# Optimization experiments

Hardware: AMD Instinct MI355X
Metric: run time of the kernel (lower is better)

The kernel has to match this reference:

```python
import jax, jax.numpy as jnp
import numpy as np

NB_USERS = 100000
NB_MOVIES = 20000
K = 64
N = 2000000
MAX_RATING = 5.0


def setup_inputs() -> dict:
    key = jax.random.key(0)
    ks = jax.random.split(key, 8)
    return {
        "x_users": jnp.arange(NB_USERS, dtype=jnp.int32),  # every user queried once -> original's user filter is identity
        "x_movies": jax.random.randint(ks[0], (NB_USERS,), 0, NB_MOVIES),
        "data_users": jax.random.randint(ks[1], (N,), 0, NB_USERS),
        "data_movies": jax.random.randint(ks[2], (N,), 0, NB_MOVIES),
        "data_ratings": jax.random.uniform(ks[3], (N,), dtype=jnp.float32) * MAX_RATING,
        "movies_features": jax.random.normal(ks[4], (NB_MOVIES, K), dtype=jnp.float32),
        "W_r": jax.random.normal(ks[5], (K, 1), dtype=jnp.float32) * 0.1,
        "b_r": jnp.zeros((K,), dtype=jnp.float32),
        "W_c": jax.random.normal(ks[6], (K, K), dtype=jnp.float32) * 0.1,
        "b_c": jnp.zeros((K,), dtype=jnp.float32),
        "w_out": jax.random.normal(ks[7], (1, 1), dtype=jnp.float32),
        "b_out": jnp.zeros((1,), dtype=jnp.float32),
    }


def reference(x_users, x_movies, data_users, data_movies, data_ratings,
              movies_features, W_r, b_r, W_c, b_c, w_out, b_out):
    # movies_ratings_func: Linear(1,k) + sigmoid on normalized ratings
    ratings = jax.nn.sigmoid((data_ratings[:, None] / MAX_RATING) @ W_r.T + b_r)  # [N,k]
    # combined_func: Linear(k,k) + sigmoid on (gathered movie feats * rating emb)
    rbm = jax.nn.sigmoid((movies_features[data_movies] * ratings) @ W_c.T + b_c)  # [N,k]
    # scatter-add aggregate per user
    rating_by_user = jax.ops.segment_sum(rbm, data_users, num_segments=NB_USERS)  # [U,k]
    nb_ratings = jax.ops.segment_sum(jnp.ones((N,), dtype=rbm.dtype), data_users,
                                     num_segments=NB_USERS)  # [U]
    # ignore_if_seen=True path (faithful, including rbm indexed by movie id as in original)
    rating_by_user = rating_by_user.at[x_users].add(-rbm[x_movies])
    nb_ratings = nb_ratings.at[x_users].set(jnp.maximum(jnp.float32(1.0), nb_ratings[x_users] - 1.0))
    user_features = rating_by_user[x_users] / nb_ratings[x_users][:, None]  # [B,k]
    movie_features = movies_features[x_movies]  # [B,k]
    r = (movie_features * user_features).mean(-1, keepdims=True)  # [B,1]
    r = (r @ w_out.T + b_out) * MAX_RATING  # result_func then *max_rating
    return r.reshape(-1)
```

## Files before the change

### kernel.cpp

```cpp
#include <hip/hip_runtime.h>

#define NB_USERS 100000
#define NB_MOVIES 20000
#define KDIM 64
#define NPTS 2000000
#define RQ_LEVELS 8192
#define UPB 128
#define NBUCK 782
#define CHUNK 8192
#define NCHUNK ((NPTS + CHUNK - 1) / CHUNK)
#define BCAP 3584
#define LOG2E 1.44269504088896f

#define MF_N (NB_MOVIES * KDIM)
#define RT_N ((RQ_LEVELS + 1) * KDIM)

typedef _Float16 f16x8 __attribute__((ext_vector_type(8)));
typedef float    f32x4 __attribute__((ext_vector_type(4)));

__device__ __forceinline__ float sigmoidf(float z) {
    return 1.0f / (1.0f + __expf(-z));
}
__device__ __forceinline__ float sigmoid_w(float w) {
    return __builtin_amdgcn_rcpf(1.0f + __builtin_amdgcn_exp2f(w));
}

__global__ __launch_bounds__(256) void prep_kernel(
    const float* __restrict__ mf, const float* __restrict__ W_r,
    const float* __restrict__ b_r, const float* __restrict__ W_c,
    _Float16* __restrict__ mf16, _Float16* __restrict__ rtab16,
    _Float16* __restrict__ wcfrag)
{
    const int idx = blockIdx.x * 256 + threadIdx.x;
    if (idx < MF_N) {
        mf16[idx] = (_Float16)mf[idx];
    } else if (idx < MF_N + RT_N) {
        const int i = idx - MF_N;
        const int q = i >> 6, k = i & 63;
        rtab16[i] = (_Float16)sigmoidf(fmaf((float)q * (1.0f / RQ_LEVELS), W_r[k], b_r[k]));
    } else if (idx < MF_N + RT_N + 512) {
        const int i = idx - MF_N - RT_N;
        const int ntkt = i >> 6;
        const int nt = ntkt >> 1, kt = ntkt & 1;
        const int lane = i & 63;
        const float* src = &W_c[(nt * 16 + (lane & 15)) * KDIM + kt * 32 + (lane >> 4) * 8];
        _Float16* dst = wcfrag + (size_t)ntkt * 512 + lane * 8;
        #pragma unroll
        for (int e = 0; e < 8; ++e) dst[e] = (_Float16)(src[e] * -LOG2E);
    }
}

__global__ __launch_bounds__(1024) void bucket_hist_kernel(
    const int* __restrict__ du, int* __restrict__ bhist)
{
    __shared__ int h[NBUCK];
    for (int b = threadIdx.x; b < NBUCK; b += 1024) h[b] = 0;
    __syncthreads();
    int i = blockIdx.x * 1024 + threadIdx.x;
    const int stride = gridDim.x * 1024;
    for (; i < NPTS; i += stride) atomicAdd(&h[du[i] >> 7], 1);
    __syncthreads();
    for (int b = threadIdx.x; b < NBUCK; b += 1024)
        if (h[b]) atomicAdd(&bhist[b], h[b]);
}

__global__ __launch_bounds__(256) void bscan_kernel(
    const int* __restrict__ bhist, int* __restrict__ bstart, int* __restrict__ bcursor)
{
    __shared__ int scn[256];
    const int t = threadIdx.x;
    int c[4];
    int s = 0;
    #pragma unroll
    for (int j = 0; j < 4; ++j) {
        const int idx = t * 4 + j;
        c[j] = (idx < NBUCK) ? bhist[idx] : 0;
        s += c[j];
    }
    scn[t] = s;
    __syncthreads();
    for (int d = 1; d < 256; d <<= 1) {
        const int a = (t >= d) ? scn[t - d] : 0;
        __syncthreads();
        scn[t] += a;
        __syncthreads();
    }
    int run = scn[t] - s;
    #pragma unroll
    for (int j = 0; j < 4; ++j) {
        const int idx = t * 4 + j;
        if (idx < NBUCK) { bstart[idx] = run; bcursor[idx] = run; }
        run += c[j];
    }
}

__global__ __launch_bounds__(1024, 2) void binA_kernel(
    const int* __restrict__ du, const int* __restrict__ dm,
    const float* __restrict__ dr,
    int* __restrict__ bcursor, uint2* __restrict__ binned)
{
    __shared__ uint2 buf[CHUNK];
    __shared__ int cnt[NBUCK];
    __shared__ int scn[1024];
    __shared__ int sbase[NBUCK];
    __shared__ int cur[NBUCK];
    __shared__ int gbase[NBUCK];

    const int t  = threadIdx.x;
    const int c0 = blockIdx.x * CHUNK;
    const int n  = min(CHUNK, NPTS - c0);

    for (int b = t; b < NBUCK; b += 1024) cnt[b] = 0;
    __syncthreads();

    for (int i = t; i < n; i += 1024)
        atomicAdd(&cnt[(unsigned)du[c0 + i] >> 7], 1);
    __syncthreads();

    const int cv = (t < NBUCK) ? cnt[t] : 0;
    scn[t] = cv;
    __syncthreads();
    for (int d = 1; d < 1024; d <<= 1) {
        const int a = (t >= d) ? scn[t - d] : 0;
        __syncthreads();
        scn[t] += a;
        __syncthreads();
    }
    if (t < NBUCK) {
        const int e = scn[t] - cv;
        sbase[t] = e;
        cur[t]   = e;
        if (cv > 0) gbase[t] = atomicAdd(&bcursor[t], cv);
    }
    __syncthreads();

    for (int i = t; i < n; i += 1024) {
        const unsigned u  = (unsigned)du[c0 + i];
        const unsigned m  = (unsigned)dm[c0 + i];
        const unsigned rq = (unsigned)(int)fmaf(dr[c0 + i], (float)RQ_LEVELS / 5.0f, 0.5f);
        const int pos = atomicAdd(&cur[u >> 7], 1);
        buf[pos] = make_uint2((u << 15) | m, rq);
    }
    __syncthreads();

    for (int i = t; i < n; i += 1024) {
        const uint2 q = buf[i];
        const int b = q.x >> 22;
        binned[gbase[b] + (i - sbase[b])] = q;
    }
}

__global__ __launch_bounds__(256) void rbm_saved_kernel(
    const int* __restrict__ dm, const float* __restrict__ dr,
    const _Float16* __restrict__ mf16, const _Float16* __restrict__ rtab16,
    const _Float16* __restrict__ wcfrag, const float* __restrict__ b_c,
    float* __restrict__ rbm_saved)
{
    __shared__ _Float16 bsh[8 * 512];
    for (int i = threadIdx.x; i < 512; i += 256)
        ((f16x8*)bsh)[i] = ((const f16x8*)wcfrag)[i];
    __syncthreads();

    const int lane = threadIdx.x & 63;
    const int wave = blockIdx.x * (blockDim.x >> 6) + (threadIdx.x >> 6);
    const int NT = (NB_MOVIES + 63) / 64;
    if (wave >= NT) return;

    float wbcv[4];
    #pragma unroll
    for (int nt = 0; nt < 4; ++nt) wbcv[nt] = -LOG2E * b_c[nt * 16 + (lane & 15)];

    const int base = wave * 64;
    const int koff = (lane >> 4) * 8;

    #pragma unroll 1
    for (int mt = 0; mt < 4; ++mt) {
        const int pg = base + mt * 16 + (lane & 15);
        int   m = 0;
        float r = 0.f;
        if (pg < NB_MOVIES) { m = dm[pg]; r = dr[pg]; }
        const int rq = (int)fmaf(r, (float)RQ_LEVELS / 5.0f, 0.5f);

        const f16x8 ma = *(const f16x8*)(mf16   + (size_t)m  * KDIM + koff);
        const f16x8 mb = *(const f16x8*)(mf16   + (size_t)m  * KDIM + 32 + koff);
        const f16x8 ta = *(const f16x8*)(rtab16 + (size_t)rq * KDIM + koff);
        const f16x8 tb = *(const f16x8*)(rtab16 + (size_t)rq * KDIM + 32 + koff);
        const f16x8 a0 = ma * ta;
        const f16x8 a1 = mb * tb;

        f32x4 acc[4];
        #pragma unroll
        for (int nt = 0; nt < 4; ++nt) {
            const f16x8 b0 = *(const f16x8*)(bsh + (nt * 2 + 0) * 512 + lane * 8);
            const f16x8 b1 = *(const f16x8*)(bsh + (nt * 2 + 1) * 512 + lane * 8);
            acc[nt] = (f32x4){0.f, 0.f, 0.f, 0.f};
            acc[nt] = __builtin_amdgcn_mfma_f32_16x16x32_f16(a0, b0, acc[nt], 0, 0, 0);
            acc[nt] = __builtin_amdgcn_mfma_f32_16x16x32_f16(a1, b1, acc[nt], 0, 0, 0);
        }

        #pragma unroll
        for (int reg = 0; reg < 4; ++reg) {
            const int prow_g = base + mt * 16 + (lane >> 4) * 4 + reg;
            if (prow_g < NB_MOVIES) {
                #pragma unroll
                for (int nt = 0; nt < 4; ++nt) {
                    const float rbm = sigmoid_w(acc[nt][reg] + wbcv[nt]);
                    rbm_saved[(size_t)prow_g * KDIM + nt * 16 + (lane & 15)] = rbm;
                }
            }
        }
    }
}

__global__ __launch_bounds__(512, 4) void phase1_fused_kernel(
    const uint2* __restrict__ binned,
    const int* __restrict__ bhist, const int* __restrict__ bstart,
    const _Float16* __restrict__ mf16,
    const _Float16* __restrict__ rtab16,
    const _Float16* __restrict__ wcfrag,
    const float* __restrict__ b_c,
    float* __restrict__ rbu, float* __restrict__ nbrf)
{
    __shared__ uint2 buf[BCAP];
    __shared__ _Float16 bsh[8 * 512];
    __shared__ int cnt[UPB];
    __shared__ int cur[UPB];

    const int t    = threadIdx.x;
    const int lane = t & 63;
    const int wid  = t >> 6;
    const int g    = lane >> 4;
    const int b    = blockIdx.x;
    const int n    = bhist[b];
    const int s0   = bstart[b];

    if (t < 512) ((f16x8*)bsh)[t] = ((const f16x8*)wcfrag)[t];
    if (t < UPB) cnt[t] = 0;

    {
        const size_t row0 = (size_t)b * UPB * KDIM;
        const size_t rows = (size_t)min(UPB, NB_USERS - b * UPB) * KDIM;
        for (size_t i = t; i < rows; i += 512) rbu[row0 + i] = 0.f;
    }
    __syncthreads();

    for (int i = t; i < n; i += 512)
        atomicAdd(&cnt[(binned[s0 + i].x >> 15) & (UPB - 1)], 1);
    __syncthreads();

    const int uid = b * UPB + t;
    if (t < UPB && uid < NB_USERS) nbrf[uid] = (float)cnt[t];

    const int inc = (t < UPB) ? cnt[t] : 0;
    if (t < UPB) cur[t] = inc;
    __syncthreads();
    for (int d = 1; d < UPB; d <<= 1) {
        const int a = (t < UPB && t >= d) ? cur[t - d] : 0;
        __syncthreads();
        if (t < UPB) cur[t] += a;
        __syncthreads();
    }
    if (t < UPB) cur[t] -= inc;
    __syncthreads();

    for (int i = t; i < n; i += 512) {
        const uint2 q  = binned[s0 + i];
        const int  lu  = (q.x >> 15) & (UPB - 1);
        const int  pos = atomicAdd(&cur[lu], 1);
        buf[pos] = q;
    }
    __syncthreads();

    float wbcv[4];
    #pragma unroll
    for (int nt = 0; nt < 4; ++nt) wbcv[nt] = -LOG2E * b_c[nt * 16 + (lane & 15)];
    const int koff = g * 8;

    const int T = (n + 63) >> 6;
    for (int tt = wid; tt < T; tt += 8) {
        const int t0 = tt * 64;

        f16x8 A0[4], A1[4];
        int   uats[4];
        #pragma unroll
        for (int mt = 0; mt < 4; ++mt) {
            const int pi = t0 + mt * 16 + (lane & 15);
            const uint2 ur = (pi < n) ? buf[pi] : make_uint2(0xFFFFFFFFu, 0u);
            uats[mt] = (int)(ur.x >> 15);
            const int m  = min((int)(ur.x & 0x7fffu), NB_MOVIES - 1);
            const int rq = (int)ur.y;

            const f16x8 ma = *(const f16x8*)(mf16   + (size_t)m  * KDIM + koff);
            const f16x8 mb = *(const f16x8*)(mf16   + (size_t)m  * KDIM + 32 + koff);
            const f16x8 ta = *(const f16x8*)(rtab16 + (size_t)rq * KDIM + koff);
            const f16x8 tb = *(const f16x8*)(rtab16 + (size_t)rq * KDIM + 32 + koff);
            A0[mt] = ma * ta;
            A1[mt] = mb * tb;
        }

        #pragma unroll
        for (int mt = 0; mt < 4; ++mt) {
            const unsigned u_at = (unsigned)uats[mt];

            f32x4 acc[4];
            #pragma unroll
            for (int nt = 0; nt < 4; ++nt) {
                const f16x8 b0 = *(const f16x8*)(bsh + (nt * 2 + 0) * 512 + lane * 8);
                const f16x8 b1 = *(const f16x8*)(bsh + (nt * 2 + 1) * 512 + lane * 8);
                acc[nt] = (f32x4){0.f, 0.f, 0.f, 0.f};
                acc[nt] = __builtin_amdgcn_mfma_f32_16x16x32_f16(A0[mt], b0, acc[nt], 0, 0, 0);
                acc[nt] = __builtin_amdgcn_mfma_f32_16x16x32_f16(A1[mt], b1, acc[nt], 0, 0, 0);
            }

            #pragma unroll
            for (int nt = 0; nt < 4; ++nt)
                #pragma unroll
                for (int reg = 0; reg < 4; ++reg)
                    acc[nt][reg] = sigmoid_w(acc[nt][reg] + wbcv[nt]);

            const unsigned u_prev = (unsigned)__shfl(uats[mt], lane - 1, 64);
            const bool boundary = ((lane & 15) == 0) || (u_at != u_prev);
            unsigned long long bm = __ballot(boundary) & 0xFFFFull;

            while (bm) {
                const int s = __builtin_ctzll(bm);
                bm &= bm - 1;
                const int e = bm ? __builtin_ctzll(bm) : 16;
                const unsigned useg =
                    (unsigned)__builtin_amdgcn_readlane(uats[mt], s);
                if (useg >= (unsigned)NB_USERS) continue;

                const int lo = s - g * 4;
                const int hi = e - g * 4;
                float p0 = 0.f, p1 = 0.f, p2 = 0.f, p3 = 0.f;
                #pragma unroll
                for (int reg = 0; reg < 4; ++reg) {
                    const bool in = (reg >= lo) && (reg < hi);
                    p0 += in ? acc[0][reg] : 0.f;
                    p1 += in ? acc[1][reg] : 0.f;
                    p2 += in ? acc[2][reg] : 0.f;
                    p3 += in ? acc[3][reg] : 0.f;
                }
                p0 += __shfl_xor(p0, 16, 64); p0 += __shfl_xor(p0, 32, 64);
                p1 += __shfl_xor(p1, 16, 64); p1 += __shfl_xor(p1, 32, 64);
                p2 += __shfl_xor(p2, 16, 64); p2 += __shfl_xor(p2, 32, 64);
                p3 += __shfl_xor(p3, 16, 64); p3 += __shfl_xor(p3, 32, 64);

                const float v01 = (g & 1) ? p1 : p0;
                const float v23 = (g & 1) ? p3 : p2;
                const float val = (g & 2) ? v23 : v01;
                atomicAdd(&rbu[(size_t)useg * KDIM + lane], val);
            }
        }
    }
}

__global__ __launch_bounds__(256) void phase2_kernel(
    const int* __restrict__ x_users,
    const int* __restrict__ x_movies,
    const float* __restrict__ mf,
    const float* __restrict__ rbu,
    const float* __restrict__ nbrf,
    const float* __restrict__ rbm_saved,
    const float* __restrict__ w_out,
    const float* __restrict__ b_out,
    float* __restrict__ out)
{
    const int lane = threadIdx.x & 63;
    const int wave = blockIdx.x * (blockDim.x >> 6) + (threadIdx.x >> 6);
    if (wave >= NB_USERS) return;

    const int u  = x_users[wave];
    const int xm = x_movies[wave];

    const float nb = fmaxf(1.0f, nbrf[u] - 1.0f);
    const float uf = (rbu[(size_t)u * KDIM + lane] -
                      rbm_saved[(size_t)xm * KDIM + lane]) / nb;
    float p = mf[(size_t)xm * KDIM + lane] * uf;

    #pragma unroll
    for (int off = 32; off > 0; off >>= 1)
        p += __shfl_xor(p, off, 64);

    if (lane == 0)
        out[wave] = (p * (1.0f / 64.0f) * w_out[0] + b_out[0]) * 5.0f;
}

extern "C" void kernel_launch(void* const* d_in, const int* in_sizes, int n_in,
                              void* d_out, int out_size, void* d_ws, size_t ws_size,
                              hipStream_t stream) {
    const int*   x_users      = (const int*)  d_in[0];
    const int*   x_movies     = (const int*)  d_in[1];
    const int*   data_users   = (const int*)  d_in[2];
    const int*   data_movies  = (const int*)  d_in[3];
    const float* data_ratings = (const float*)d_in[4];
    const float* mf           = (const float*)d_in[5];
    const float* W_r          = (const float*)d_in[6];
    const float* b_r          = (const float*)d_in[7];
    const float* W_c          = (const float*)d_in[8];
    const float* b_c          = (const float*)d_in[9];
    const float* w_out        = (const float*)d_in[10];
    const float* b_out        = (const float*)d_in[11];
    float* out = (float*)d_out;

    float*     rbu       = (float*)d_ws;
    float*     nbrf      = rbu + (size_t)NB_USERS * KDIM;
    float*     rbm_saved = nbrf + NB_USERS;
    uint2*     binned    = (uint2*)(rbm_saved + (size_t)NB_MOVIES * KDIM);
    _Float16*  mf16      = (_Float16*)(binned + NPTS);
    _Float16*  rtab16    = mf16 + (size_t)MF_N;
    _Float16*  wcfrag    = rtab16 + (size_t)RT_N;
    int*       bhist     = (int*)(wcfrag + 8 * 512);
    int*       bstart    = bhist + NBUCK;
    int*       bcursor   = bstart + NBUCK;

    hipMemsetAsync(bhist, 0, NBUCK * sizeof(int), stream);

    prep_kernel<<<(MF_N + RT_N + 512 + 255) / 256, 256, 0, stream>>>(
        mf, W_r, b_r, W_c, mf16, rtab16, wcfrag);

    bucket_hist_kernel<<<512, 1024, 0, stream>>>(data_users, bhist);
    bscan_kernel<<<1, 256, 0, stream>>>(bhist, bstart, bcursor);

    binA_kernel<<<NCHUNK, 1024, 0, stream>>>(
        data_users, data_movies, data_ratings, bcursor, binned);

    rbm_saved_kernel<<<79, 256, 0, stream>>>(
        data_movies, data_ratings, mf16, rtab16, wcfrag, b_c, rbm_saved);

    phase1_fused_kernel<<<NBUCK, 512, 0, stream>>>(
        binned, bhist, bstart, mf16, rtab16, wcfrag, b_c, rbu, nbrf);

    phase2_kernel<<<(NB_USERS * 64 + 255) / 256, 256, 0, stream>>>(
        x_users, x_movies, mf, rbu, nbrf, rbm_saved, w_out, b_out, out);
}
```

Baseline: 177.7 us.

## Split per-bucket sort from MFMA phase into separate globally-sorted pass

```diff
diff --git a/kernel.cpp b/kernel.cpp
--- a/kernel.cpp
+++ b/kernel.cpp
@@ -4,6 +4,7 @@
 #define NB_MOVIES 20000
 #define KDIM 64
 #define NPTS 2000000
+#define NTILES (NPTS / 64)
 #define RQ_LEVELS 8192
 #define UPB 128
 #define NBUCK 782
@@ -150,6 +151,54 @@
     }
 }
 
+__global__ __launch_bounds__(256) void binB_kernel(
+    const uint2* __restrict__ binned,
+    const int* __restrict__ bhist, const int* __restrict__ bstart,
+    uint2* __restrict__ sorted, float* __restrict__ nbrf)
+{
+    __shared__ uint2 buf[BCAP];
+    __shared__ int cnt[UPB];
+    __shared__ int cur[UPB];
+
+    const int t  = threadIdx.x;
+    const int b  = blockIdx.x;
+    const int n  = bhist[b];
+    const int s0 = bstart[b];
+
+    if (t < UPB) cnt[t] = 0;
+    __syncthreads();
+
+    for (int i = t; i < n; i += 256)
+        atomicAdd(&cnt[(binned[s0 + i].x >> 15) & (UPB - 1)], 1);
+    __syncthreads();
+
+    const int uid = b * UPB + t;
+    if (t < UPB && uid < NB_USERS) nbrf[uid] = (float)cnt[t];
+
+    const int inc = (t < UPB) ? cnt[t] : 0;
+    if (t < UPB) cur[t] = inc;
+    __syncthreads();
+    for (int d = 1; d < UPB; d <<= 1) {
+        const int a = (t < UPB && t >= d) ? cur[t - d] : 0;
+        __syncthreads();
+        if (t < UPB) cur[t] += a;
+        __syncthreads();
+    }
+    if (t < UPB) cur[t] -= inc;
+    __syncthreads();
+
+    for (int i = t; i < n; i += 256) {
+        const uint2 q  = binned[s0 + i];
+        const int  lu  = (q.x >> 15) & (UPB - 1);
+        const int  pos = atomicAdd(&cur[lu], 1);
+        buf[pos] = q;
+    }
+    __syncthreads();
+
+    for (int i = t; i < n; i += 256)
+        sorted[s0 + i] = buf[i];
+}
+
 __global__ __launch_bounds__(256) void rbm_saved_kernel(
     const int* __restrict__ dm, const float* __restrict__ dr,
     const _Float16* __restrict__ mf16, const _Float16* __restrict__ rtab16,
@@ -212,95 +261,46 @@
     }
 }
 
-__global__ __launch_bounds__(512, 4) void phase1_fused_kernel(
-    const uint2* __restrict__ binned,
-    const int* __restrict__ bhist, const int* __restrict__ bstart,
+__global__ __launch_bounds__(256, 4) void phase1_sorted_kernel(
+    const uint2* __restrict__ sorted_ur,
     const _Float16* __restrict__ mf16,
     const _Float16* __restrict__ rtab16,
     const _Float16* __restrict__ wcfrag,
     const float* __restrict__ b_c,
-    float* __restrict__ rbu, float* __restrict__ nbrf)
-{
-    __shared__ uint2 buf[BCAP];
+    float* __restrict__ rbu)
+{
     __shared__ _Float16 bsh[8 * 512];
-    __shared__ int cnt[UPB];
-    __shared__ int cur[UPB];
-
-    const int t    = threadIdx.x;
-    const int lane = t & 63;
-    const int wid  = t >> 6;
-    const int g    = lane >> 4;
-    const int b    = blockIdx.x;
-    const int n    = bhist[b];
-    const int s0   = bstart[b];
-
-    if (t < 512) ((f16x8*)bsh)[t] = ((const f16x8*)wcfrag)[t];
-    if (t < UPB) cnt[t] = 0;
-
-    {
-        const size_t row0 = (size_t)b * UPB * KDIM;
-        const size_t rows = (size_t)min(UPB, NB_USERS - b * UPB) * KDIM;
-        for (size_t i = t; i < rows; i += 512) rbu[row0 + i] = 0.f;
-    }
-    __syncthreads();
-
-    for (int i = t; i < n; i += 512)
-        atomicAdd(&cnt[(binned[s0 + i].x >> 15) & (UPB - 1)], 1);
-    __syncthreads();
-
-    const int uid = b * UPB + t;
-    if (t < UPB && uid < NB_USERS) nbrf[uid] = (float)cnt[t];
-
-    const int inc = (t < UPB) ? cnt[t] : 0;
-    if (t < UPB) cur[t] = inc;
-    __syncthreads();
-    for (int d = 1; d < UPB; d <<= 1) {
-        const int a = (t < UPB && t >= d) ? cur[t - d] : 0;
-        __syncthreads();
-        if (t < UPB) cur[t] += a;
-        __syncthreads();
-    }
-    if (t < UPB) cur[t] -= inc;
-    __syncthreads();
-
-    for (int i = t; i < n; i += 512) {
-        const uint2 q  = binned[s0 + i];
-        const int  lu  = (q.x >> 15) & (UPB - 1);
-        const int  pos = atomicAdd(&cur[lu], 1);
-        buf[pos] = q;
-    }
-    __syncthreads();
+    for (int i = threadIdx.x; i < 512; i += 256)
+        ((f16x8*)bsh)[i] = ((const f16x8*)wcfrag)[i];
+    __syncthreads();
+
+    const int lane = threadIdx.x & 63;
+    const int wave = blockIdx.x * (blockDim.x >> 6) + (threadIdx.x >> 6);
+    const int nwav = gridDim.x * (blockDim.x >> 6);
 
     float wbcv[4];
     #pragma unroll
     for (int nt = 0; nt < 4; ++nt) wbcv[nt] = -LOG2E * b_c[nt * 16 + (lane & 15)];
-    const int koff = g * 8;
-
-    const int T = (n + 63) >> 6;
-    for (int tt = wid; tt < T; tt += 8) {
-        const int t0 = tt * 64;
-
-        f16x8 A0[4], A1[4];
-        int   uats[4];
-        #pragma unroll
+
+    const int koff = (lane >> 4) * 8;
+    const int g    = lane >> 4;
+
+    for (int it = wave; it < NTILES; it += nwav) {
+        const int base = it * 64;
+
+        #pragma unroll 1
         for (int mt = 0; mt < 4; ++mt) {
-            const int pi = t0 + mt * 16 + (lane & 15);
-            const uint2 ur = (pi < n) ? buf[pi] : make_uint2(0xFFFFFFFFu, 0u);
-            uats[mt] = (int)(ur.x >> 15);
-            const int m  = min((int)(ur.x & 0x7fffu), NB_MOVIES - 1);
-            const int rq = (int)ur.y;
+            const uint2 ur = sorted_ur[base + mt * 16 + (lane & 15)];
+            const unsigned u_at = ur.x >> 15;
+            const int      m    = (int)(ur.x & 0x7fffu);
+            const int      rq   = (int)ur.y;
 
             const f16x8 ma = *(const f16x8*)(mf16   + (size_t)m  * KDIM + koff);
             const f16x8 mb = *(const f16x8*)(mf16   + (size_t)m  * KDIM + 32 + koff);
             const f16x8 ta = *(const f16x8*)(rtab16 + (size_t)rq * KDIM + koff);
             const f16x8 tb = *(const f16x8*)(rtab16 + (size_t)rq * KDIM + 32 + koff);
-            A0[mt] = ma * ta;
-            A1[mt] = mb * tb;
-        }
-
-        #pragma unroll
-        for (int mt = 0; mt < 4; ++mt) {
-            const unsigned u_at = (unsigned)uats[mt];
+            const f16x8 a0 = ma * ta;
+            const f16x8 a1 = mb * tb;
 
             f32x4 acc[4];
             #pragma unroll
@@ -308,8 +308,8 @@
                 const f16x8 b0 = *(const f16x8*)(bsh + (nt * 2 + 0) * 512 + lane * 8);
                 const f16x8 b1 = *(const f16x8*)(bsh + (nt * 2 + 1) * 512 + lane * 8);
                 acc[nt] = (f32x4){0.f, 0.f, 0.f, 0.f};
-                acc[nt] = __builtin_amdgcn_mfma_f32_16x16x32_f16(A0[mt], b0, acc[nt], 0, 0, 0);
-                acc[nt] = __builtin_amdgcn_mfma_f32_16x16x32_f16(A1[mt], b1, acc[nt], 0, 0, 0);
+                acc[nt] = __builtin_amdgcn_mfma_f32_16x16x32_f16(a0, b0, acc[nt], 0, 0, 0);
+                acc[nt] = __builtin_amdgcn_mfma_f32_16x16x32_f16(a1, b1, acc[nt], 0, 0, 0);
             }
 
             #pragma unroll
@@ -318,7 +318,8 @@
                 for (int reg = 0; reg < 4; ++reg)
                     acc[nt][reg] = sigmoid_w(acc[nt][reg] + wbcv[nt]);
 
-            const unsigned u_prev = (unsigned)__shfl(uats[mt], lane - 1, 64);
+            const unsigned u_prev =
+                (unsigned)__shfl((int)u_at, lane - 1, 64);
             const bool boundary = ((lane & 15) == 0) || (u_at != u_prev);
             unsigned long long bm = __ballot(boundary) & 0xFFFFull;
 
@@ -327,8 +328,7 @@
                 bm &= bm - 1;
                 const int e = bm ? __builtin_ctzll(bm) : 16;
                 const unsigned useg =
-                    (unsigned)__builtin_amdgcn_readlane(uats[mt], s);
-                if (useg >= (unsigned)NB_USERS) continue;
+                    (unsigned)__builtin_amdgcn_readlane((int)u_at, s);
 
                 const int lo = s - g * 4;
                 const int hi = e - g * 4;
@@ -404,10 +404,11 @@
     float* out = (float*)d_out;
 
     float*     rbu       = (float*)d_ws;
+    uint2*     binned    = (uint2*)d_ws;
     float*     nbrf      = rbu + (size_t)NB_USERS * KDIM;
     float*     rbm_saved = nbrf + NB_USERS;
-    uint2*     binned    = (uint2*)(rbm_saved + (size_t)NB_MOVIES * KDIM);
-    _Float16*  mf16      = (_Float16*)(binned + NPTS);
+    uint2*     sorted_ur = (uint2*)(rbm_saved + (size_t)NB_MOVIES * KDIM);
+    _Float16*  mf16      = (_Float16*)(sorted_ur + NPTS);
     _Float16*  rtab16    = mf16 + (size_t)MF_N;
     _Float16*  wcfrag    = rtab16 + (size_t)RT_N;
     int*       bhist     = (int*)(wcfrag + 8 * 512);
@@ -428,8 +429,12 @@
     rbm_saved_kernel<<<79, 256, 0, stream>>>(
         data_movies, data_ratings, mf16, rtab16, wcfrag, b_c, rbm_saved);
 
-    phase1_fused_kernel<<<NBUCK, 512, 0, stream>>>(
-        binned, bhist, bstart, mf16, rtab16, wcfrag, b_c, rbu, nbrf);
+    binB_kernel<<<NBUCK, 256, 0, stream>>>(binned, bhist, bstart, sorted_ur, nbrf);
+
+    hipMemsetAsync(rbu, 0, (size_t)NB_USERS * KDIM * sizeof(float), stream);
+
+    phase1_sorted_kernel<<<2048, 256, 0, stream>>>(
+        sorted_ur, mf16, rtab16, wcfrag, b_c, rbu);
 
     phase2_kernel<<<(NB_USERS * 64 + 255) / 256, 256, 0, stream>>>(
         x_users, x_movies, mf, rbu, nbrf, rbm_saved, w_out, b_out, out);
```

Result: faster. 169.9 us (-4.4%).
